# Performance work log

Measured on AMD Instinct MI355X. Metric: run time of the kernel, lower is better.

Reference implementation:

```python
import jax, jax.numpy as jnp
import numpy as np

V, S, D, H = 32000, 1024, 768, 3072
EPS = 1e-5


def pos_encoding(seq_len, dim, dtype=jnp.float32):
    # pe[pos, i] = sin(pos/10000^(i/dim)) if i even else cos(pos/10000^(i/dim))
    pos = jnp.arange(seq_len, dtype=dtype)[:, None]
    i = jnp.arange(dim, dtype=dtype)[None, :]
    ang = pos / jnp.power(jnp.asarray(10000.0, dtype), i / dim)
    even = (jnp.arange(dim) % 2 == 0)[None, :]
    return jnp.where(even, jnp.sin(ang), jnp.cos(ang))


def layernorm2d(x, w, b):
    # normalizes over last two dims (token_size, input_dim), affine params [S, D]
    m = jnp.mean(x, axis=(-2, -1), keepdims=True)
    v = jnp.mean((x - m) ** 2, axis=(-2, -1), keepdims=True)
    return (x - m) / jnp.sqrt(v + EPS) * w + b


def setup_inputs() -> dict:
    key = jax.random.key(0)
    ks = jax.random.split(key, 16)
    sc = 0.02
    emb = jax.random.normal(ks[0], (V, D), jnp.float32) * sc
    emb = emb.at[0].set(0.0)  # padding_idx=0
    inp = {
        "x": jax.random.randint(ks[1], (8, S), 0, V),
        "emb": emb,
        "Wq": jax.random.normal(ks[2], (D, H), jnp.float32) * sc,
        "bq": jnp.zeros((H,), jnp.float32),
        "Wk": jax.random.normal(ks[3], (D, H), jnp.float32) * sc,
        "bk": jnp.zeros((H,), jnp.float32),
        "Wv": jax.random.normal(ks[4], (D, H), jnp.float32) * sc,
        "bv": jnp.zeros((H,), jnp.float32),
        "Wo": jax.random.normal(ks[5], (H, D), jnp.float32) * sc,
        "bo": jnp.zeros((D,), jnp.float32),
        "W1": jax.random.normal(ks[6], (D, H), jnp.float32) * sc,
        "b1": jnp.zeros((H,), jnp.float32),
        "W2": jax.random.normal(ks[7], (H, D), jnp.float32) * sc,
        "b2": jnp.zeros((D,), jnp.float32),
        "ln1_w": jnp.ones((S, D), jnp.float32),
        "ln1_b": jnp.zeros((S, D), jnp.float32),
        "ln2_w": jnp.ones((S, D), jnp.float32),
        "ln2_b": jnp.zeros((S, D), jnp.float32),
    }
    return inp


def reference(x, emb, Wq, bq, Wk, bk, Wv, bv, Wo, bo, W1, b1, W2, b2, ln1_w, ln1_b, ln2_w, ln2_b):
    y = emb[x]                                   # [B, S, D]
    y = y + pos_encoding(y.shape[1], y.shape[2], y.dtype)
    # unscaled self-attention (no 1/sqrt(d) factor, faithful to source)
    q = y @ Wq + bq
    k = y @ Wk + bk
    v = y @ Wv + bv
    attn = jax.nn.softmax(jnp.einsum("bsh,bth->bst", q, k), axis=-1)
    a = jnp.einsum("bst,bth->bsh", attn, v) @ Wo + bo
    y = layernorm2d(y + a, ln1_w, ln1_b)
    # FFN: GELU applied AFTER second linear (faithful to source)
    f = jax.nn.gelu((y @ W1 + b1) @ W2 + b2, approximate=False)
    y = layernorm2d(y + f, ln2_w, ln2_b)
    return y
```

## Files before the change

kernel.cpp:

```cpp
#include <hip/hip_runtime.h>
#include <hip/hip_fp16.h>

#define DI __device__ __forceinline__

typedef _Float16 f16x8 __attribute__((ext_vector_type(8)));
typedef float f32x4 __attribute__((ext_vector_type(4)));

struct alignas(8) h4 { __half x, y, z, w; };

DI void async16(const void* g, void* l) {
  __builtin_amdgcn_global_load_lds(
      (__attribute__((address_space(1))) void*)g,
      (__attribute__((address_space(3))) void*)l, 16, 0, 0);
}

DI float waveReduceSum(float v) {
#pragma unroll
  for (int i = 1; i < 64; i <<= 1) v += __shfl_xor(v, i);
  return v;
}
DI float waveReduceMax(float v) {
#pragma unroll
  for (int i = 1; i < 64; i <<= 1) v = fmaxf(v, __shfl_xor(v, i));
  return v;
}

DI float gelu_exact(float x) { return 0.5f * x * (1.f + erff(x * 0.70710678118654752f)); }

template <typename CT, bool BIAS, bool BROW>
__global__ __launch_bounds__(256) void gemm_nt(
    const __half* __restrict__ A, int lda, long long sA,
    const __half* __restrict__ Bt, int ldb, long long sB,
    const float* __restrict__ bias, long long sBias,
    CT* __restrict__ C, int ldc, long long sC,
    int bandN, int nb, int gm, int K) {
  __shared__ __align__(16) __half As[128 * 64];
  __shared__ __align__(16) __half Bs[128 * 64];

  const int tid = threadIdx.x;
  const int wave = tid >> 6, lane = tid & 63;

  const int xcd = blockIdx.x & 7;
  const int j = blockIdx.x >> 3;
  const int per = nb * gm;
  const int grp = j / per, rem = j - grp * per;
  int m, n;
  if (bandN) { m = grp * gm + rem % gm; n = xcd * nb + rem / gm; }
  else       { n = grp * gm + rem % gm; m = xcd * nb + rem / gm; }
  const int m0 = m * 128, n0 = n * 128;

  A += (long long)blockIdx.z * sA;
  Bt += (long long)blockIdx.z * sB;
  C += (long long)blockIdx.z * sC;
  if constexpr (BIAS || BROW) bias += (long long)blockIdx.z * sBias;
  const int wm = wave & 1, wn = wave >> 1;

  f32x4 acc[4][4];
#pragma unroll
  for (int i = 0; i < 4; ++i)
#pragma unroll
    for (int jj = 0; jj < 4; ++jj) acc[i][jj] = (f32x4){0.f, 0.f, 0.f, 0.f};

  const int srow = tid >> 3;
  const int gc = (tid & 7) ^ (srow & 7);
  const __half* Ag = A + (size_t)(m0 + srow) * lda + gc * 8;
  const __half* Bg = Bt + (size_t)(n0 + srow) * ldb + gc * 8;
  const size_t a32 = (size_t)32 * lda, b32 = (size_t)32 * ldb;
  char* AsW = (char*)As + wave * 1024;
  char* BsW = (char*)Bs + wave * 1024;

  const int ml = lane & 15, q = lane >> 4, lx = lane & 7;

  for (int k0 = 0; k0 < K; k0 += 64) {
#pragma unroll
    for (int i = 0; i < 4; ++i) {
      async16(Ag + i * a32 + k0, AsW + i * 4096);
      async16(Bg + i * b32 + k0, BsW + i * 4096);
    }
    __syncthreads();
#pragma unroll
    for (int jj = 0; jj < 2; ++jj) {
      f16x8 af[4], bf[4];
#pragma unroll
      for (int i = 0; i < 4; ++i) {
        af[i] = *(const f16x8*)(As + ((size_t)(wm * 64 + i * 16 + ml) * 8 + ((q + 4 * jj) ^ lx)) * 8);
        bf[i] = *(const f16x8*)(Bs + ((size_t)(wn * 64 + i * 16 + ml) * 8 + ((q + 4 * jj) ^ lx)) * 8);
      }
#pragma unroll
      for (int i = 0; i < 4; ++i)
#pragma unroll
        for (int jn = 0; jn < 4; ++jn)
          acc[i][jn] = __builtin_amdgcn_mfma_f32_16x16x32_f16(af[i], bf[jn], acc[i][jn], 0, 0, 0);
    }
    __syncthreads();
  }

#pragma unroll
  for (int jj = 0; jj < 4; ++jj) {
    const int col = n0 + wn * 64 + jj * 16 + ml;
    const float bcol = BIAS ? bias[col] : 0.f;
#pragma unroll
    for (int i = 0; i < 4; ++i) {
      const int row = m0 + wm * 64 + i * 16 + q * 4;
#pragma unroll
      for (int rr = 0; rr < 4; ++rr) {
        float v = acc[i][jj][rr] + bcol;
        if constexpr (BROW) v += bias[row + rr];
        if constexpr (sizeof(CT) == 4)
          C[(size_t)(row + rr) * ldc + col] = v;
        else
          C[(size_t)(row + rr) * ldc + col] = __float2half(v);
      }
    }
  }
}

__global__ __launch_bounds__(256) void prep1(
    const float* __restrict__ Wq, const float* __restrict__ Wk,
    const float* __restrict__ Wv, const float* __restrict__ W1,
    const float* __restrict__ bq, const float* __restrict__ bk,
    __half* __restrict__ wA, __half* __restrict__ wB, __half* __restrict__ wC,
    float* __restrict__ bqk) {
  if (blockIdx.x == 2304) {
    if (blockIdx.y == 0)
      for (int i = threadIdx.x; i < 3072; i += 256) {
        bqk[i] = bq[i];
        bqk[3072 + i] = bk[i];
      }
    return;
  }
  const float* in;
  __half* out;
  switch (blockIdx.y) {
    case 0: in = Wq; out = wA; break;
    case 1: in = Wk; out = wA + 3072 * 768; break;
    case 2: in = Wv; out = wB; break;
    default: in = W1; out = wC; break;
  }
  __shared__ float t[32][33];
  const int tx = threadIdx.x & 31, ty = threadIdx.x >> 5;
  const int cb = blockIdx.x % 96, rb = blockIdx.x / 96;
  const int c = cb * 32 + tx, r0 = rb * 32;
#pragma unroll
  for (int i = 0; i < 32; i += 8) t[ty + i][tx] = in[(size_t)(r0 + ty + i) * 3072 + c];
  __syncthreads();
  const int oc = r0 + tx, o0 = cb * 32;
#pragma unroll
  for (int i = 0; i < 32; i += 8)
    out[(size_t)(o0 + ty + i) * 768 + oc] = __float2half(t[tx][ty + i]);
}

__global__ __launch_bounds__(256) void prep2(
    const float* __restrict__ Wo, const float* __restrict__ W2, __half* __restrict__ wA) {
  const float* in = blockIdx.y ? W2 : Wo;
  __half* out = wA + (blockIdx.y ? 3072 * 768 : 0);
  __shared__ float t[32][33];
  const int tx = threadIdx.x & 31, ty = threadIdx.x >> 5;
  const int cb = blockIdx.x % 24, rb = blockIdx.x / 24;
  const int c = cb * 32 + tx, r0 = rb * 32;
#pragma unroll
  for (int i = 0; i < 32; i += 8) t[ty + i][tx] = in[(size_t)(r0 + ty + i) * 768 + c];
  __syncthreads();
  const int oc = r0 + tx, o0 = cb * 32;
#pragma unroll
  for (int i = 0; i < 32; i += 8)
    out[(size_t)(o0 + ty + i) * 3072 + oc] = __float2half(t[tx][ty + i]);
}

__global__ __launch_bounds__(256) void embed_pos_kernel(
    const int* __restrict__ x, const float* __restrict__ emb,
    float* __restrict__ y, __half* __restrict__ yh) {
  const int row = blockIdx.x;
  const int s = row & 1023;
  const int tok = x[row];
  const float* ep = emb + (size_t)tok * 768;
  float* yp = y + (size_t)row * 768;
  __half* hp = yh + (size_t)row * 768;
  const float c = -13.287712379549449f / 768.f;
  for (int d = threadIdx.x; d < 768; d += 256) {
    float ang = (float)s * exp2f((float)d * c);
    float pe = (d & 1) ? cosf(ang) : sinf(ang);
    float v = ep[d] + pe;
    yp[d] = v;
    hp[d] = __float2half(v);
  }
}

__global__ __launch_bounds__(256) void softmax_rows(
    const float* __restrict__ L, __half* __restrict__ P) {
  const size_t row = blockIdx.x;
  const float4 x = ((const float4*)(L + row * 1024))[threadIdx.x];
  const int wave = threadIdx.x >> 6, lane = threadIdx.x & 63;
  float m = fmaxf(fmaxf(x.x, x.y), fmaxf(x.z, x.w));
  m = waveReduceMax(m);
  __shared__ float sm[4];
  __shared__ float ssum[4];
  if (lane == 0) sm[wave] = m;
  __syncthreads();
  m = fmaxf(fmaxf(sm[0], sm[1]), fmaxf(sm[2], sm[3]));
  float e0 = expf(x.x - m), e1 = expf(x.y - m), e2 = expf(x.z - m), e3 = expf(x.w - m);
  float s = e0 + e1 + e2 + e3;
  s = waveReduceSum(s);
  if (lane == 0) ssum[wave] = s;
  __syncthreads();
  s = ssum[0] + ssum[1] + ssum[2] + ssum[3];
  const float inv = 1.f / s;
  h4 o{__float2half(e0 * inv), __float2half(e1 * inv), __float2half(e2 * inv),
       __float2half(e3 * inv)};
  ((h4*)(P + row * 1024))[threadIdx.x] = o;
}

template <bool GELU>
__global__ __launch_bounds__(256) void residual_stats(
    float* __restrict__ y, const float* __restrict__ p0, const float* __restrict__ p1,
    const float* __restrict__ bias, float2* __restrict__ partials) {
  const int b = blockIdx.y, chunk = blockIdx.x;
  const size_t base = (size_t)b * 786432 + (size_t)chunk * 8192;
  float4* yp = (float4*)(y + base);
  const float4* a0 = (const float4*)(p0 + base);
  const float4* a1 = (const float4*)(p1 + base);
  float s = 0.f, ss = 0.f;
#pragma unroll
  for (int it = 0; it < 8; ++it) {
    const int idx = it * 256 + threadIdx.x;
    const int d = (chunk * 8192 + it * 1024 + threadIdx.x * 4) % 768;
    float4 yv = yp[idx];
    float4 v0 = a0[idx];
    float4 v1 = a1[idx];
    const float4 bv = *(const float4*)(bias + d);
    float ax = v0.x + v1.x + bv.x, ay = v0.y + v1.y + bv.y;
    float az = v0.z + v1.z + bv.z, aw = v0.w + v1.w + bv.w;
    if constexpr (GELU) {
      ax = gelu_exact(ax); ay = gelu_exact(ay);
      az = gelu_exact(az); aw = gelu_exact(aw);
    }
    float4 r{yv.x + ax, yv.y + ay, yv.z + az, yv.w + aw};
    yp[idx] = r;
    s += r.x + r.y + r.z + r.w;
    ss += r.x * r.x + r.y * r.y + r.z * r.z + r.w * r.w;
  }
  s = waveReduceSum(s);
  ss = waveReduceSum(ss);
  __shared__ float2 wr[4];
  const int wave = threadIdx.x >> 6, lane = threadIdx.x & 63;
  if (lane == 0) wr[wave] = make_float2(s, ss);
  __syncthreads();
  if (threadIdx.x == 0) {
    float S = wr[0].x + wr[1].x + wr[2].x + wr[3].x;
    float SS = wr[0].y + wr[1].y + wr[2].y + wr[3].y;
    partials[b * 96 + chunk] = make_float2(S, SS);
  }
}

template <bool WB>
__global__ __launch_bounds__(256) void ln_apply(
    float* __restrict__ y, __half* __restrict__ yh, const float* __restrict__ w,
    const float* __restrict__ bb, const float2* __restrict__ partials) {
  const unsigned i4 = blockIdx.x * 256 + threadIdx.x;
  const unsigned i = i4 * 4;
  const unsigned b = i / 786432u;
  const int tid = threadIdx.x;
  float s = 0.f, ss = 0.f;
  if (tid < 96) {
    float2 p = partials[b * 96 + tid];
    s = p.x;
    ss = p.y;
  }
  s = waveReduceSum(s);
  ss = waveReduceSum(ss);
  __shared__ float2 wsum[4];
  if ((tid & 63) == 0) wsum[tid >> 6] = make_float2(s, ss);
  __syncthreads();
  const float S = wsum[0].x + wsum[1].x + wsum[2].x + wsum[3].x;
  const float SS = wsum[0].y + wsum[1].y + wsum[2].y + wsum[3].y;
  const float inv = 1.f / 786432.f;
  const float mean = S * inv;
  const float rstd = rsqrtf(SS * inv - mean * mean + 1e-5f);

  const unsigned e4 = (i - b * 786432u) >> 2;
  float4 yv = ((const float4*)y)[i4];
  const float4 wv = ((const float4*)w)[e4];
  const float4 bv = ((const float4*)bb)[e4];
  float4 r;
  r.x = (yv.x - mean) * rstd * wv.x + bv.x;
  r.y = (yv.y - mean) * rstd * wv.y + bv.y;
  r.z = (yv.z - mean) * rstd * wv.z + bv.z;
  r.w = (yv.w - mean) * rstd * wv.w + bv.w;
  ((float4*)y)[i4] = r;
  if constexpr (WB) {
    h4 o{__float2half(r.x), __float2half(r.y), __float2half(r.z), __float2half(r.w)};
    ((h4*)yh)[i4] = o;
  }
}

extern "C" void kernel_launch(void* const* d_in, const int* in_sizes, int n_in,
                              void* d_out, int out_size, void* d_ws, size_t ws_size,
                              hipStream_t stream) {
  const int* x = (const int*)d_in[0];
  const float* emb = (const float*)d_in[1];
  const float* Wq = (const float*)d_in[2];
  const float* bq = (const float*)d_in[3];
  const float* Wk = (const float*)d_in[4];
  const float* bk = (const float*)d_in[5];
  const float* Wv = (const float*)d_in[6];
  const float* bv = (const float*)d_in[7];
  const float* Wo = (const float*)d_in[8];
  const float* bo = (const float*)d_in[9];
  const float* W1 = (const float*)d_in[10];
  const float* b1 = (const float*)d_in[11];
  const float* W2 = (const float*)d_in[12];
  const float* b2 = (const float*)d_in[13];
  const float* ln1w = (const float*)d_in[14];
  const float* ln1b = (const float*)d_in[15];
  const float* ln2w = (const float*)d_in[16];
  const float* ln2b = (const float*)d_in[17];

  float* y = (float*)d_out;

  char* ws = (char*)d_ws;
  __half* yh = (__half*)(ws + 0);
  __half* qb = (__half*)(ws + 12582912);
  __half* kb = (__half*)(ws + 62914560);
  __half* Ph = kb;
  __half* vT = (__half*)(ws + 113246208);
  float* abuf = (float*)vT;
  float* Lg = (float*)(ws + 163577856);
  __half* wA = (__half*)(ws + 197132288);
  __half* wB = (__half*)(ws + 206569472);
  __half* wC = (__half*)(ws + 211288064);
  float* bqk = (float*)(ws + 216006656);
  float2* part = (float2*)(ws + 216031232);
  const size_t WS_NEEDED = 216037440;
  if (ws_size < WS_NEEDED) return;

  const dim3 blk(256);
  const long long SH = 1024LL * 3072, SS = 1024LL * 1024;
  const long long HALF = 25165824;
  float* p1 = abuf + 6291456;

  prep1<<<dim3(2305, 4), blk, 0, stream>>>(Wq, Wk, Wv, W1, bq, bk, wA, wB, wC, bqk);
  embed_pos_kernel<<<dim3(8192), blk, 0, stream>>>(x, emb, y, yh);

  gemm_nt<__half, true, false><<<dim3(1536, 1, 2), blk, 0, stream>>>(
      yh, 768, 0, wA, 768, 3072LL * 768, bqk, 3072, qb, 3072, HALF, 1, 3, 8, 768);
  prep2<<<dim3(2304, 2), blk, 0, stream>>>(Wo, W2, wA);

  gemm_nt<__half, false, true><<<dim3(192, 1, 8), blk, 0, stream>>>(
      wB, 768, 0, yh, 768, 1024LL * 768, bv, 0, vT, 1024, SH, 0, 3, 8, 768);

  gemm_nt<float, false, false><<<dim3(64, 1, 8), blk, 0, stream>>>(
      qb, 3072, SH, kb, 3072, SH, nullptr, 0, Lg, 1024, SS, 1, 1, 8, 3072);

  softmax_rows<<<dim3(8192), blk, 0, stream>>>(Lg, Ph);

  gemm_nt<__half, false, false><<<dim3(192, 1, 8), blk, 0, stream>>>(
      Ph, 1024, SS, vT, 1024, SH, nullptr, 0, (__half*)qb, 3072, SH, 1, 3, 8, 1024);

  gemm_nt<float, false, false><<<dim3(384, 1, 2), blk, 0, stream>>>(
      (__half*)qb, 3072, 1536, wA, 3072, 1536, nullptr, 0, abuf, 768, 6291456, 0, 8, 6, 1536);

  residual_stats<false><<<dim3(96, 8), blk, 0, stream>>>(y, abuf, p1, bo, part);
  ln_apply<true><<<dim3(6144), blk, 0, stream>>>(y, yh, ln1w, ln1b, part);

  gemm_nt<__half, true, false><<<dim3(1536, 1, 1), blk, 0, stream>>>(
      yh, 768, 0, wC, 768, 0, b1, 0, (__half*)qb, 3072, 0, 1, 3, 8, 768);
  gemm_nt<float, false, false><<<dim3(384, 1, 2), blk, 0, stream>>>(
      (__half*)qb, 3072, 1536, wA + 3072 * 768, 3072, 1536, nullptr, 0, abuf, 768, 6291456, 0, 8, 6, 1536);

  residual_stats<true><<<dim3(96, 8), blk, 0, stream>>>(y, abuf, p1, b2, part);
  ln_apply<false><<<dim3(6144), blk, 0, stream>>>(y, nullptr, ln2w, ln2b, part);
}
```

Measured before the change: 749.4 us.

## Simplify GEMM tile mapping, precompute LDS offsets, merge weight prep kernels

Replaces the XCD-aware banded block-to-tile mapping in the GEMM with a simple grouped raster: eight consecutive M tiles share one N tile. It also precomputes swizzled LDS read offsets so the fragment loads use constant strides and an XOR. Separately, it merges the two weight transpose/convert kernels into one launch by giving Wo/W2 their own workspace region, so the QK weights no longer share a buffer that had to be overwritten between GEMMs. This saves a launch and some address arithmetic, but may lose the L2 locality the XCD-aware mapping provided on the multi-die MI355X.

After: 729.7 us. 2.6% less time.

```diff
diff --git a/kernel.cpp b/kernel.cpp
--- a/kernel.cpp
+++ b/kernel.cpp
@@ -33,21 +33,17 @@
     const __half* __restrict__ Bt, int ldb, long long sB,
     const float* __restrict__ bias, long long sBias,
     CT* __restrict__ C, int ldc, long long sC,
-    int bandN, int nb, int gm, int K) {
+    int nT, int K) {
   __shared__ __align__(16) __half As[128 * 64];
   __shared__ __align__(16) __half Bs[128 * 64];
 
   const int tid = threadIdx.x;
   const int wave = tid >> 6, lane = tid & 63;
 
-  const int xcd = blockIdx.x & 7;
-  const int j = blockIdx.x >> 3;
-  const int per = nb * gm;
-  const int grp = j / per, rem = j - grp * per;
-  int m, n;
-  if (bandN) { m = grp * gm + rem % gm; n = xcd * nb + rem / gm; }
-  else       { n = grp * gm + rem % gm; m = xcd * nb + rem / gm; }
-  const int m0 = m * 128, n0 = n * 128;
+  const int gsz = 8 * nT;
+  const int g = blockIdx.x / gsz, r = blockIdx.x % gsz;
+  const int m0 = (g * 8 + (r & 7)) * 128;
+  const int n0 = (r >> 3) * 128;
 
   A += (long long)blockIdx.z * sA;
   Bt += (long long)blockIdx.z * sB;
@@ -70,6 +66,8 @@
   char* BsW = (char*)Bs + wave * 1024;
 
   const int ml = lane & 15, q = lane >> 4, lx = lane & 7;
+  const int aoff = ((wm * 64 + ml) * 8 + (q ^ lx)) * 16;
+  const int boff = ((wn * 64 + ml) * 8 + (q ^ lx)) * 16;
 
   for (int k0 = 0; k0 < K; k0 += 64) {
 #pragma unroll
@@ -80,11 +78,13 @@
     __syncthreads();
 #pragma unroll
     for (int jj = 0; jj < 2; ++jj) {
+      const char* Ab = (const char*)As + (jj ? (aoff ^ 64) : aoff);
+      const char* Bb = (const char*)Bs + (jj ? (boff ^ 64) : boff);
       f16x8 af[4], bf[4];
 #pragma unroll
       for (int i = 0; i < 4; ++i) {
-        af[i] = *(const f16x8*)(As + ((size_t)(wm * 64 + i * 16 + ml) * 8 + ((q + 4 * jj) ^ lx)) * 8);
-        bf[i] = *(const f16x8*)(Bs + ((size_t)(wn * 64 + i * 16 + ml) * 8 + ((q + 4 * jj) ^ lx)) * 8);
+        af[i] = *(const f16x8*)(Ab + i * 2048);
+        bf[i] = *(const f16x8*)(Bb + i * 2048);
       }
 #pragma unroll
       for (int i = 0; i < 4; ++i)
@@ -115,12 +115,13 @@
   }
 }
 
-__global__ __launch_bounds__(256) void prep1(
+__global__ __launch_bounds__(256) void prep(
     const float* __restrict__ Wq, const float* __restrict__ Wk,
     const float* __restrict__ Wv, const float* __restrict__ W1,
+    const float* __restrict__ Wo, const float* __restrict__ W2,
     const float* __restrict__ bq, const float* __restrict__ bk,
-    __half* __restrict__ wA, __half* __restrict__ wB, __half* __restrict__ wC,
-    float* __restrict__ bqk) {
+    __half* __restrict__ wD, __half* __restrict__ wB, __half* __restrict__ wC,
+    __half* __restrict__ wA, float* __restrict__ bqk) {
   if (blockIdx.x == 2304) {
     if (blockIdx.y == 0)
       for (int i = threadIdx.x; i < 3072; i += 256) {
@@ -129,42 +130,39 @@
       }
     return;
   }
-  const float* in;
-  __half* out;
-  switch (blockIdx.y) {
-    case 0: in = Wq; out = wA; break;
-    case 1: in = Wk; out = wA + 3072 * 768; break;
-    case 2: in = Wv; out = wB; break;
-    default: in = W1; out = wC; break;
-  }
   __shared__ float t[32][33];
   const int tx = threadIdx.x & 31, ty = threadIdx.x >> 5;
-  const int cb = blockIdx.x % 96, rb = blockIdx.x / 96;
-  const int c = cb * 32 + tx, r0 = rb * 32;
-#pragma unroll
-  for (int i = 0; i < 32; i += 8) t[ty + i][tx] = in[(size_t)(r0 + ty + i) * 3072 + c];
-  __syncthreads();
-  const int oc = r0 + tx, o0 = cb * 32;
-#pragma unroll
-  for (int i = 0; i < 32; i += 8)
-    out[(size_t)(o0 + ty + i) * 768 + oc] = __float2half(t[tx][ty + i]);
-}
-
-__global__ __launch_bounds__(256) void prep2(
-    const float* __restrict__ Wo, const float* __restrict__ W2, __half* __restrict__ wA) {
-  const float* in = blockIdx.y ? W2 : Wo;
-  __half* out = wA + (blockIdx.y ? 3072 * 768 : 0);
-  __shared__ float t[32][33];
-  const int tx = threadIdx.x & 31, ty = threadIdx.x >> 5;
-  const int cb = blockIdx.x % 24, rb = blockIdx.x / 24;
-  const int c = cb * 32 + tx, r0 = rb * 32;
-#pragma unroll
-  for (int i = 0; i < 32; i += 8) t[ty + i][tx] = in[(size_t)(r0 + ty + i) * 768 + c];
-  __syncthreads();
-  const int oc = r0 + tx, o0 = cb * 32;
-#pragma unroll
-  for (int i = 0; i < 32; i += 8)
-    out[(size_t)(o0 + ty + i) * 3072 + oc] = __float2half(t[tx][ty + i]);
+  if (blockIdx.y < 4) {
+    const float* in;
+    __half* out;
+    switch (blockIdx.y) {
+      case 0: in = Wq; out = wD; break;
+      case 1: in = Wk; out = wD + 3072 * 768; break;
+      case 2: in = Wv; out = wB; break;
+      default: in = W1; out = wC; break;
+    }
+    const int cb = blockIdx.x % 96, rb = blockIdx.x / 96;
+    const int c = cb * 32 + tx, r0 = rb * 32;
+#pragma unroll
+    for (int i = 0; i < 32; i += 8) t[ty + i][tx] = in[(size_t)(r0 + ty + i) * 3072 + c];
+    __syncthreads();
+    const int oc = r0 + tx, o0 = cb * 32;
+#pragma unroll
+    for (int i = 0; i < 32; i += 8)
+      out[(size_t)(o0 + ty + i) * 768 + oc] = __float2half(t[tx][ty + i]);
+  } else {
+    const float* in = (blockIdx.y == 5) ? W2 : Wo;
+    __half* out = wA + ((blockIdx.y == 5) ? 3072 * 768 : 0);
+    const int cb = blockIdx.x % 24, rb = blockIdx.x / 24;
+    const int c = cb * 32 + tx, r0 = rb * 32;
+#pragma unroll
+    for (int i = 0; i < 32; i += 8) t[ty + i][tx] = in[(size_t)(r0 + ty + i) * 768 + c];
+    __syncthreads();
+    const int oc = r0 + tx, o0 = cb * 32;
+#pragma unroll
+    for (int i = 0; i < 32; i += 8)
+      out[(size_t)(o0 + ty + i) * 3072 + oc] = __float2half(t[tx][ty + i]);
+  }
 }
 
 __global__ __launch_bounds__(256) void embed_pos_kernel(
@@ -326,11 +324,12 @@
   float* abuf = (float*)vT;
   float* Lg = (float*)(ws + 163577856);
   __half* wA = (__half*)(ws + 197132288);
-  __half* wB = (__half*)(ws + 206569472);
-  __half* wC = (__half*)(ws + 211288064);
-  float* bqk = (float*)(ws + 216006656);
-  float2* part = (float2*)(ws + 216031232);
-  const size_t WS_NEEDED = 216037440;
+  __half* wD = (__half*)(ws + 206569472);
+  __half* wB = (__half*)(ws + 216006656);
+  __half* wC = (__half*)(ws + 220725248);
+  float* bqk = (float*)(ws + 225443840);
+  float2* part = (float2*)(ws + 225468416);
+  const size_t WS_NEEDED = 225474624;
   if (ws_size < WS_NEEDED) return;
 
   const dim3 blk(256);
@@ -338,34 +337,33 @@
   const long long HALF = 25165824;
   float* p1 = abuf + 6291456;
 
-  prep1<<<dim3(2305, 4), blk, 0, stream>>>(Wq, Wk, Wv, W1, bq, bk, wA, wB, wC, bqk);
+  prep<<<dim3(2305, 6), blk, 0, stream>>>(Wq, Wk, Wv, W1, Wo, W2, bq, bk, wD, wB, wC, wA, bqk);
   embed_pos_kernel<<<dim3(8192), blk, 0, stream>>>(x, emb, y, yh);
 
   gemm_nt<__half, true, false><<<dim3(1536, 1, 2), blk, 0, stream>>>(
-      yh, 768, 0, wA, 768, 3072LL * 768, bqk, 3072, qb, 3072, HALF, 1, 3, 8, 768);
-  prep2<<<dim3(2304, 2), blk, 0, stream>>>(Wo, W2, wA);
+      yh, 768, 0, wD, 768, 3072LL * 768, bqk, 3072, qb, 3072, HALF, 24, 768);
 
   gemm_nt<__half, false, true><<<dim3(192, 1, 8), blk, 0, stream>>>(
-      wB, 768, 0, yh, 768, 1024LL * 768, bv, 0, vT, 1024, SH, 0, 3, 8, 768);
+      wB, 768, 0, yh, 768, 1024LL * 768, bv, 0, vT, 1024, SH, 8, 768);
 
   gemm_nt<float, false, false><<<dim3(64, 1, 8), blk, 0, stream>>>(
-      qb, 3072, SH, kb, 3072, SH, nullptr, 0, Lg, 1024, SS, 1, 1, 8, 3072);
+      qb, 3072, SH, kb, 3072, SH, nullptr, 0, Lg, 1024, SS, 8, 3072);
 
   softmax_rows<<<dim3(8192), blk, 0, stream>>>(Lg, Ph);
 
   gemm_nt<__half, false, false><<<dim3(192, 1, 8), blk, 0, stream>>>(
-      Ph, 1024, SS, vT, 1024, SH, nullptr, 0, (__half*)qb, 3072, SH, 1, 3, 8, 1024);
+      Ph, 1024, SS, vT, 1024, SH, nullptr, 0, (__half*)qb, 3072, SH, 24, 1024);
 
   gemm_nt<float, false, false><<<dim3(384, 1, 2), blk, 0, stream>>>(
-      (__half*)qb, 3072, 1536, wA, 3072, 1536, nullptr, 0, abuf, 768, 6291456, 0, 8, 6, 1536);
+      (__half*)qb, 3072, 1536, wA, 3072, 1536, nullptr, 0, abuf, 768, 6291456, 6, 1536);
 
   residual_stats<false><<<dim3(96, 8), blk, 0, stream>>>(y, abuf, p1, bo, part);
   ln_apply<true><<<dim3(6144), blk, 0, stream>>>(y, yh, ln1w, ln1b, part);
 
   gemm_nt<__half, true, false><<<dim3(1536, 1, 1), blk, 0, stream>>>(
-      yh, 768, 0, wC, 768, 0, b1, 0, (__half*)qb, 3072, 0, 1, 3, 8, 768);
+      yh, 768, 0, wC, 768, 0, b1, 0, (__half*)qb, 3072, 0, 24, 768);
   gemm_nt<float, false, false><<<dim3(384, 1, 2), blk, 0, stream>>>(
-      (__half*)qb, 3072, 1536, wA + 3072 * 768, 3072, 1536, nullptr, 0, abuf, 768, 6291456, 0, 8, 6, 1536);
+      (__half*)qb, 3072, 1536, wA + 3072 * 768, 3072, 1536, nullptr, 0, abuf, 768, 6291456, 6, 1536);
 
   residual_stats<true><<<dim3(96, 8), blk, 0, stream>>>(y, abuf, p1, b2, part);
   ln_apply<false><<<dim3(6144), blk, 0, stream>>>(y, nullptr, ln2w, ln2b, part);
```
